# Kernel tuning notes

Measured on AMD Instinct MI355X. Metric: run time of the kernel, lower is better.

## Reference

```python
import jax, jax.numpy as jnp
import numpy as np

B, L, E, H, EXP = 2, 2048, 1024, 16, 4
D = E // H
EPS = 1e-5

def layernorm(x, g, b):
    mu = jnp.mean(x, axis=-1, keepdims=True)
    var = jnp.var(x, axis=-1, keepdims=True)
    return (x - mu) * jax.lax.rsqrt(var + EPS) * g + b

def setup_inputs() -> dict:
    key = jax.random.key(0)
    ks = jax.random.split(key, 12)
    s = 0.02
    return {
        "x": jax.random.normal(ks[0], (B, L, E), dtype=jnp.float32),
        "ln1_g": jnp.ones((E,), jnp.float32),
        "ln1_b": jnp.zeros((E,), jnp.float32),
        "W_qkv": jax.random.normal(ks[1], (E, 3 * E), dtype=jnp.float32) * s,
        "W_proj": jax.random.normal(ks[2], (E, E), dtype=jnp.float32) * s,
        "b_proj": jnp.zeros((E,), jnp.float32),
        "ln2_g": jnp.ones((E,), jnp.float32),
        "ln2_b": jnp.zeros((E,), jnp.float32),
        "W1": jax.random.normal(ks[3], (E, EXP * E), dtype=jnp.float32) * s,
        "b1": jnp.zeros((EXP * E,), jnp.float32),
        "W2": jax.random.normal(ks[4], (EXP * E, E), dtype=jnp.float32) * s,
        "b2": jnp.zeros((E,), jnp.float32),
    }

def reference(x, ln1_g, ln1_b, W_qkv, W_proj, b_proj, ln2_g, ln2_b, W1, b1, W2, b2):
    # --- attention sub-block (pre-LN) ---
    h = layernorm(x, ln1_g, ln1_b)                      # [B,L,E]
    qkv = h @ W_qkv                                      # [B,L,3E]
    q, k, v = jnp.split(qkv, 3, axis=-1)
    q = q.reshape(B, L, H, D).transpose(0, 2, 1, 3)      # [B,H,L,D]
    k = k.reshape(B, L, H, D).transpose(0, 2, 1, 3)
    v = v.reshape(B, L, H, D).transpose(0, 2, 1, 3)
    scale = jnp.sqrt(jnp.float32(E))                     # NOTE: module divides by sqrt(E), not sqrt(D)
    att = jnp.einsum('bhqd,bhkd->bhqk', q, k) / scale
    att = jax.nn.softmax(att, axis=-1)
    out = jnp.einsum('bhqk,bhkd->bhqd', att, v)          # [B,H,L,D]
    out = out.transpose(0, 2, 1, 3).reshape(B, L, E)
    x = x + out @ W_proj + b_proj                         # residual
    # --- feed-forward sub-block (pre-LN) ---
    h = layernorm(x, ln2_g, ln2_b)
    h = jax.nn.gelu(h @ W1 + b1, approximate=False)       # torch GELU is exact erf
    x = x + h @ W2 + b2
    return x
```

## Files before the change

### kernel.cpp

```cpp
#include <hip/hip_runtime.h>
#include <cstdint>
#include <cstddef>


typedef __bf16 bht;
typedef __attribute__((ext_vector_type(8))) __bf16 bf16x8;
typedef __attribute__((ext_vector_type(4))) __bf16 bf16x4;
typedef __attribute__((ext_vector_type(4))) float f32x4;
typedef __attribute__((ext_vector_type(4))) short short4v;

#define B_ 2
#define L_ 2048
#define E_ 1024
#define H_ 16
#define D_ 64
#define ROWS_ (B_ * L_)

#define QSCALE_ 0.045084441f

__device__ __forceinline__ void glds16(const void* g, void* l) {
    __builtin_amdgcn_global_load_lds(
        (const __attribute__((address_space(1))) unsigned int*)g,
        (__attribute__((address_space(3))) unsigned int*)l, 16, 0, 0);
}

__device__ __forceinline__ short4v as_s4(bf16x4 v) {
    return __builtin_bit_cast(short4v, v);
}

__global__ __launch_bounds__(256)
void transpose_cast(const float* __restrict__ in, bht* __restrict__ out, int R, int C) {
    __shared__ float tile[32][33];
    const int bx = blockIdx.x * 32;
    const int by = blockIdx.y * 32;
    const int tx = threadIdx.x, ty = threadIdx.y;
    #pragma unroll
    for (int i = 0; i < 32; i += 8)
        tile[ty + i][tx] = in[(size_t)(by + ty + i) * C + bx + tx];
    __syncthreads();
    #pragma unroll
    for (int i = 0; i < 32; i += 8)
        out[(size_t)(bx + ty + i) * R + by + tx] = (bht)tile[tx][ty + i];
}

__global__ __launch_bounds__(256)
void ln_kernel(const float* __restrict__ x, const float* __restrict__ g,
               const float* __restrict__ b, bht* __restrict__ out) {
    const int row = blockIdx.x, t = threadIdx.x;
    const float4 v = ((const float4*)(x + (size_t)row * E_))[t];
    float s  = v.x + v.y + v.z + v.w;
    float ss = v.x*v.x + v.y*v.y + v.z*v.z + v.w*v.w;
    #pragma unroll
    for (int off = 32; off > 0; off >>= 1) {
        s  += __shfl_down(s, off);
        ss += __shfl_down(ss, off);
    }
    __shared__ float red[8];
    const int wave = t >> 6, lane = t & 63;
    if (lane == 0) { red[wave] = s; red[4 + wave] = ss; }
    __syncthreads();
    s  = red[0] + red[1] + red[2] + red[3];
    ss = red[4] + red[5] + red[6] + red[7];
    const float mean = s * (1.0f / (float)E_);
    const float var  = ss * (1.0f / (float)E_) - mean * mean;
    const float rstd = rsqrtf(var + 1e-5f);
    const float4 gv = ((const float4*)g)[t];
    const float4 bv = ((const float4*)b)[t];
    bf16x4 o;
    o.x = (bht)((v.x - mean) * rstd * gv.x + bv.x);
    o.y = (bht)((v.y - mean) * rstd * gv.y + bv.y);
    o.z = (bht)((v.z - mean) * rstd * gv.z + bv.z);
    o.w = (bht)((v.w - mean) * rstd * gv.w + bv.w);
    *(bf16x4*)(out + (size_t)row * E_ + t * 4) = o;
}

enum { EPI_QKV = 0, EPI_RESID = 1, EPI_GELU = 2 };

template <int EPI>
__global__ __launch_bounds__(256)
void gemm_bt(const bht* __restrict__ A, const bht* __restrict__ Bt,
             const float* __restrict__ bias, const float* __restrict__ resid,
             void* __restrict__ outp,
             bht* __restrict__ qo, bht* __restrict__ ko, bht* __restrict__ vto,
             int M, int N, int K) {
    __shared__ __align__(16) char smem[33792];
    bht* As = (bht*)smem;
    bht* Bs = (bht*)(smem + 16384);
    const int t = threadIdx.x;
    const int lane = t & 63, wave = t >> 6;
    const int lane15 = lane & 15, quad = lane >> 4;
    const int waveM = wave >> 1, waveN = wave & 1;
    const int bm = blockIdx.y * 128, bn = blockIdx.x * 128;

    f32x4 acc[4][4];
    #pragma unroll
    for (int i = 0; i < 4; ++i)
        #pragma unroll
        for (int j = 0; j < 4; ++j)
            acc[i][j] = f32x4{0.f, 0.f, 0.f, 0.f};

    const int swz = lane15 & 7;

    for (int k0 = 0; k0 < K; k0 += 64) {
        #pragma unroll
        for (int i = 0; i < 4; ++i) {
            const int g = i * 256 + t;
            const int row = g >> 3;
            const int col = ((g & 7) ^ (row & 7)) * 8;
            glds16(A  + (size_t)(bm + row) * K + k0 + col, (char*)As + (size_t)g * 16);
            glds16(Bt + (size_t)(bn + row) * K + k0 + col, (char*)Bs + (size_t)g * 16);
        }
        __syncthreads();
        #pragma unroll
        for (int kk = 0; kk < 2; ++kk) {
            const int pc = ((kk * 4 + quad) ^ swz) * 8;
            bf16x8 af[4], bfv[4];
            #pragma unroll
            for (int i = 0; i < 4; ++i)
                af[i] = *(const bf16x8*)(As + (waveM * 64 + i * 16 + lane15) * 64 + pc);
            #pragma unroll
            for (int j = 0; j < 4; ++j)
                bfv[j] = *(const bf16x8*)(Bs + (waveN * 64 + j * 16 + lane15) * 64 + pc);
            #pragma unroll
            for (int i = 0; i < 4; ++i)
                #pragma unroll
                for (int j = 0; j < 4; ++j)
                    acc[i][j] = __builtin_amdgcn_mfma_f32_16x16x32_bf16(af[i], bfv[j], acc[i][j], 0, 0, 0);
        }
        __syncthreads();
    }

    if constexpr (EPI == EPI_QKV) {
        if (bn >= 2048) {
            bht* Vtile = (bht*)smem;
            #pragma unroll
            for (int i = 0; i < 4; ++i) {
                const int rl0 = waveM * 64 + i * 16 + quad * 4;
                #pragma unroll
                for (int j = 0; j < 4; ++j) {
                    const int cl = waveN * 64 + j * 16 + lane15;
                    #pragma unroll
                    for (int r = 0; r < 4; ++r)
                        Vtile[(size_t)cl * 132 + rl0 + r] = (bht)acc[i][j][r];
                }
            }
            __syncthreads();
            const int b = bm >> 11;
            const int l0 = bm & 2047;
            #pragma unroll
            for (int it = 0; it < 8; ++it) {
                const int row = it * 16 + (t >> 4);
                const int ch  = t & 15;
                const int cg = (bn - 2048) + row;
                const int h = cg >> 6, d = cg & 63;
                const int bh = b * H_ + h;
                *(bf16x8*)(vto + ((size_t)bh * D_ + d) * L_ + l0 + ch * 8) =
                    *(const bf16x8*)(Vtile + (size_t)row * 132 + ch * 8);
            }
        } else {
            #pragma unroll
            for (int i = 0; i < 4; ++i) {
                const int row0 = bm + waveM * 64 + i * 16 + quad * 4;
                #pragma unroll
                for (int j = 0; j < 4; ++j) {
                    const int col = bn + waveN * 64 + j * 16 + lane15;
                    const int seg = col >> 10;
                    const int c = col & 1023;
                    const int h = c >> 6, d = c & 63;
                    #pragma unroll
                    for (int r = 0; r < 4; ++r) {
                        const int m = row0 + r;
                        const int b = m >> 11, l = m & 2047;
                        const int bh = b * H_ + h;
                        const float v = acc[i][j][r];
                        if (seg == 0)
                            qo[((size_t)bh * L_ + l) * D_ + d] = (bht)(v * QSCALE_);
                        else
                            ko[((size_t)bh * L_ + l) * D_ + d] = (bht)v;
                    }
                }
            }
        }
    } else {
        #pragma unroll
        for (int i = 0; i < 4; ++i) {
            const int row0 = bm + waveM * 64 + i * 16 + quad * 4;
            #pragma unroll
            for (int j = 0; j < 4; ++j) {
                const int col = bn + waveN * 64 + j * 16 + lane15;
                #pragma unroll
                for (int r = 0; r < 4; ++r) {
                    const int m = row0 + r;
                    float v = acc[i][j][r];
                    if (EPI == EPI_RESID) {
                        ((float*)outp)[(size_t)m * N + col] =
                            v + bias[col] + resid[(size_t)m * N + col];
                    } else {
                        v += bias[col];
                        v = 0.5f * v * (1.0f + erff(v * 0.70710678118654752f));
                        ((bht*)outp)[(size_t)m * N + col] = (bht)v;
                    }
                }
            }
        }
    }
}

template <int EPI>
__global__ __launch_bounds__(256)
void gemm_bt64(const bht* __restrict__ A, const bht* __restrict__ Bt,
               const float* __restrict__ bias, const float* __restrict__ resid,
               void* __restrict__ outp, int M, int N, int K) {
    __shared__ __align__(16) bht As[64 * 64];
    __shared__ __align__(16) bht Bs[128 * 64];
    const int t = threadIdx.x;
    const int lane = t & 63, wave = t >> 6;
    const int lane15 = lane & 15, quad = lane >> 4;
    const int waveM = wave >> 1, waveN = wave & 1;
    const int bm = blockIdx.y * 64, bn = blockIdx.x * 128;

    f32x4 acc[2][4];
    #pragma unroll
    for (int i = 0; i < 2; ++i)
        #pragma unroll
        for (int j = 0; j < 4; ++j)
            acc[i][j] = f32x4{0.f, 0.f, 0.f, 0.f};

    const int swz = lane15 & 7;

    for (int k0 = 0; k0 < K; k0 += 64) {
        #pragma unroll
        for (int i = 0; i < 2; ++i) {
            const int g = i * 256 + t;
            const int row = g >> 3;
            const int col = ((g & 7) ^ (row & 7)) * 8;
            glds16(A + (size_t)(bm + row) * K + k0 + col, (char*)As + (size_t)g * 16);
        }
        #pragma unroll
        for (int i = 0; i < 4; ++i) {
            const int g = i * 256 + t;
            const int row = g >> 3;
            const int col = ((g & 7) ^ (row & 7)) * 8;
            glds16(Bt + (size_t)(bn + row) * K + k0 + col, (char*)Bs + (size_t)g * 16);
        }
        __syncthreads();
        #pragma unroll
        for (int kk = 0; kk < 2; ++kk) {
            const int pc = ((kk * 4 + quad) ^ swz) * 8;
            bf16x8 af[2], bfv[4];
            #pragma unroll
            for (int i = 0; i < 2; ++i)
                af[i] = *(const bf16x8*)(As + (waveM * 32 + i * 16 + lane15) * 64 + pc);
            #pragma unroll
            for (int j = 0; j < 4; ++j)
                bfv[j] = *(const bf16x8*)(Bs + (waveN * 64 + j * 16 + lane15) * 64 + pc);
            #pragma unroll
            for (int i = 0; i < 2; ++i)
                #pragma unroll
                for (int j = 0; j < 4; ++j)
                    acc[i][j] = __builtin_amdgcn_mfma_f32_16x16x32_bf16(af[i], bfv[j], acc[i][j], 0, 0, 0);
        }
        __syncthreads();
    }

    #pragma unroll
    for (int i = 0; i < 2; ++i) {
        const int row0 = bm + waveM * 32 + i * 16 + quad * 4;
        #pragma unroll
        for (int j = 0; j < 4; ++j) {
            const int col = bn + waveN * 64 + j * 16 + lane15;
            #pragma unroll
            for (int r = 0; r < 4; ++r) {
                const int m = row0 + r;
                float v = acc[i][j][r];
                if (EPI == EPI_RESID) {
                    ((float*)outp)[(size_t)m * N + col] =
                        v + bias[col] + resid[(size_t)m * N + col];
                } else {
                    v += bias[col];
                    v = 0.5f * v * (1.0f + erff(v * 0.70710678118654752f));
                    ((bht*)outp)[(size_t)m * N + col] = (bht)v;
                }
            }
        }
    }
}

#define KT_ 128

__global__ __launch_bounds__(256)
void attn_kernel(const bht* __restrict__ Q, const bht* __restrict__ Kb,
                 const bht* __restrict__ Vt, bht* __restrict__ O) {
    __shared__ __align__(16) bht Ks[KT_ * 64];
    __shared__ __align__(16) bht Vs[64 * KT_];
    __shared__ float Ls[4][16];
    const int t = threadIdx.x;
    const int lane = t & 63, wave = t >> 6;
    const int lane15 = lane & 15, quad = lane >> 4;
    const int bh = blockIdx.x, qt = blockIdx.y;

    const bht* Qh = Q  + (size_t)bh * L_ * D_;
    const bht* Kh = Kb + (size_t)bh * L_ * D_;
    const bht* Vh = Vt + (size_t)bh * D_ * L_;

    const int q0 = qt * 64 + wave * 16;

    bf16x8 aq[2];
    #pragma unroll
    for (int kc = 0; kc < 2; ++kc)
        aq[kc] = *(const bf16x8*)(Qh + (size_t)(q0 + lane15) * D_ + kc * 32 + quad * 8);

    f32x4 o_acc[4];
    #pragma unroll
    for (int db = 0; db < 4; ++db) o_acc[db] = f32x4{0.f, 0.f, 0.f, 0.f};
    float l_sum = 0.f;

    const int pc0 = (quad ^ (lane15 & 7)) * 8;
    const int pc1 = pc0 ^ 32;

    for (int kt = 0; kt < L_ / KT_; ++kt) {
        const int key0 = kt * KT_;
        #pragma unroll
        for (int i = 0; i < 4; ++i) {
            const int g = i * 256 + t;
            const int krow = g >> 3;
            const int ksc = ((g & 7) ^ (krow & 7)) * 8;
            glds16(Kh + (size_t)(key0 + krow) * D_ + ksc, (char*)Ks + (size_t)g * 16);
        }
        #pragma unroll
        for (int i = 0; i < 4; ++i) {
            const int g = i * 256 + t;
            const int vrow = g >> 4;
            const int vsc = ((g & 15) ^ (vrow & 7)) * 8;
            glds16(Vh + (size_t)vrow * L_ + key0 + vsc, (char*)Vs + (size_t)g * 16);
        }
        __syncthreads();

        #pragma unroll
        for (int nb = 0; nb < 8; ++nb) {
            const bf16x8 ak0 = *(const bf16x8*)(Ks + (nb * 16 + lane15) * 64 + pc0);
            const bf16x8 ak1 = *(const bf16x8*)(Ks + (nb * 16 + lane15) * 64 + pc1);
            f32x4 st = __builtin_amdgcn_mfma_f32_16x16x32_bf16(
                ak0, aq[0], f32x4{0.f, 0.f, 0.f, 0.f}, 0, 0, 0);
            st = __builtin_amdgcn_mfma_f32_16x16x32_bf16(ak1, aq[1], st, 0, 0, 0);
            bf16x4 pk;
            #pragma unroll
            for (int r = 0; r < 4; ++r) {
                const float pv = exp2f(st[r]);
                l_sum += pv;
                pk[r] = (bht)pv;
            }
            const short4v pf = as_s4(pk);
            #pragma unroll
            for (int db = 0; db < 4; ++db) {
                const int row = db * 16 + lane15;
                const int c16 = (nb * 2 + (quad >> 1)) ^ (row & 7);
                const bf16x4 bv = *(const bf16x4*)(Vs + row * KT_ + c16 * 8 + (quad & 1) * 4);
                o_acc[db] = __builtin_amdgcn_mfma_f32_16x16x16bf16_1k(
                    pf, as_s4(bv), o_acc[db], 0, 0, 0);
            }
        }
        __syncthreads();
    }

    l_sum += __shfl_xor(l_sum, 16);
    l_sum += __shfl_xor(l_sum, 32);
    Ls[wave][lane15] = l_sum;
    asm volatile("s_waitcnt lgkmcnt(0)" ::: "memory");

    const int b = bh >> 4, h = bh & 15;
    #pragma unroll
    for (int r = 0; r < 4; ++r) {
        const int l = q0 + quad * 4 + r;
        const float inv = 1.0f / Ls[wave][quad * 4 + r];
        #pragma unroll
        for (int db = 0; db < 4; ++db)
            O[((size_t)b * L_ + l) * E_ + h * 64 + db * 16 + lane15] =
                (bht)(o_acc[db][r] * inv);
    }
}

extern "C" void kernel_launch(void* const* d_in, const int* in_sizes, int n_in,
                              void* d_out, int out_size, void* d_ws, size_t ws_size,
                              hipStream_t stream) {
    const float* x      = (const float*)d_in[0];
    const float* ln1_g  = (const float*)d_in[1];
    const float* ln1_b  = (const float*)d_in[2];
    const float* W_qkv  = (const float*)d_in[3];
    const float* W_proj = (const float*)d_in[4];
    const float* b_proj = (const float*)d_in[5];
    const float* ln2_g  = (const float*)d_in[6];
    const float* ln2_b  = (const float*)d_in[7];
    const float* W1     = (const float*)d_in[8];
    const float* b1     = (const float*)d_in[9];
    const float* W2     = (const float*)d_in[10];
    const float* b2     = (const float*)d_in[11];
    float* out = (float*)d_out;

    char* ws = (char*)d_ws;
    auto alloc = [&](size_t bytes) {
        char* p = ws;
        ws += (bytes + 255) & ~(size_t)255;
        return p;
    };
    bht*   WqkvT  = (bht*)alloc((size_t)3072 * 1024 * 2);
    bht*   WprojT = (bht*)alloc((size_t)1024 * 1024 * 2);
    bht*   W1T    = (bht*)alloc((size_t)4096 * 1024 * 2);
    bht*   W2T    = (bht*)alloc((size_t)1024 * 4096 * 2);
    bht*   hb     = (bht*)alloc((size_t)ROWS_ * E_ * 2);
    float* x1     = (float*)alloc((size_t)ROWS_ * E_ * 4);
    bht*   Qb     = (bht*)alloc((size_t)B_ * H_ * L_ * D_ * 2);
    bht*   Kbuf   = (bht*)alloc((size_t)B_ * H_ * L_ * D_ * 2);
    bht*   Vtb    = (bht*)alloc((size_t)B_ * H_ * D_ * L_ * 2);
    bht*   attno  = (bht*)alloc((size_t)ROWS_ * E_ * 2);
    bht*   ffn1   = Qb;

    transpose_cast<<<dim3(3072 / 32, 1024 / 32), dim3(32, 8), 0, stream>>>(W_qkv, WqkvT, 1024, 3072);
    transpose_cast<<<dim3(1024 / 32, 1024 / 32), dim3(32, 8), 0, stream>>>(W_proj, WprojT, 1024, 1024);
    transpose_cast<<<dim3(4096 / 32, 1024 / 32), dim3(32, 8), 0, stream>>>(W1, W1T, 1024, 4096);
    transpose_cast<<<dim3(1024 / 32, 4096 / 32), dim3(32, 8), 0, stream>>>(W2, W2T, 4096, 1024);

    ln_kernel<<<ROWS_, 256, 0, stream>>>(x, ln1_g, ln1_b, hb);

    gemm_bt<EPI_QKV><<<dim3(3072 / 128, ROWS_ / 128), 256, 0, stream>>>(
        hb, WqkvT, nullptr, nullptr, nullptr, Qb, Kbuf, Vtb, ROWS_, 3072, 1024);

    attn_kernel<<<dim3(B_ * H_, L_ / 64), 256, 0, stream>>>(Qb, Kbuf, Vtb, attno);

    gemm_bt64<EPI_RESID><<<dim3(1024 / 128, ROWS_ / 64), 256, 0, stream>>>(
        attno, WprojT, b_proj, x, x1, ROWS_, 1024, 1024);

    ln_kernel<<<ROWS_, 256, 0, stream>>>(x1, ln2_g, ln2_b, hb);

    gemm_bt<EPI_GELU><<<dim3(4096 / 128, ROWS_ / 128), 256, 0, stream>>>(
        hb, W1T, b1, nullptr, ffn1, nullptr, nullptr, nullptr, ROWS_, 4096, 1024);

    gemm_bt64<EPI_RESID><<<dim3(1024 / 128, ROWS_ / 64), 256, 0, stream>>>(
        ffn1, W2T, b2, x1, out, ROWS_, 1024, 4096);

    (void)in_sizes; (void)n_in; (void)out_size; (void)ws_size;
}
```

Measured before the change: 388.6 us.

## Overlap next K/V tile loads with attention compute and swizzle V halves

Splits each attention key tile into a QK/softmax phase and a PV phase. The next K tile is prefetched while PV runs and the next V tile while the following QK phase runs, with explicit waitcnt/barriers and raised wave priority around the MFMA sections. The V-transpose store swaps 4-element halves for half the threads and the PV read applies a matching XOR on the half offset, to reduce LDS bank conflicts. This adds more barriers per tile and holds 8 packed P fragments in registers, which raises register pressure.

```diff
diff --git a/kernel.cpp b/kernel.cpp
--- a/kernel.cpp
+++ b/kernel.cpp
@@ -154,8 +154,10 @@
                 const int cg = (bn - 2048) + row;
                 const int h = cg >> 6, d = cg & 63;
                 const int bh = b * H_ + h;
-                *(bf16x8*)(vto + ((size_t)bh * D_ + d) * L_ + l0 + ch * 8) =
-                    *(const bf16x8*)(Vtile + (size_t)row * 132 + ch * 8);
+                bf16x8 vv = *(const bf16x8*)(Vtile + (size_t)row * 132 + ch * 8);
+                if (t & 128)
+                    vv = __builtin_shufflevector(vv, vv, 4, 5, 6, 7, 0, 1, 2, 3);
+                *(bf16x8*)(vto + ((size_t)bh * D_ + d) * L_ + l0 + ch * 8) = vv;
             }
         } else {
             #pragma unroll
@@ -287,6 +289,7 @@
 }
 
 #define KT_ 128
+#define NT_ (L_ / KT_)
 
 __global__ __launch_bounds__(256)
 void attn_kernel(const bht* __restrict__ Q, const bht* __restrict__ Kb,
@@ -317,9 +320,10 @@
 
     const int pc0 = (quad ^ (lane15 & 7)) * 8;
     const int pc1 = pc0 ^ 32;
-
-    for (int kt = 0; kt < L_ / KT_; ++kt) {
-        const int key0 = kt * KT_;
+    const int vhalf4 = ((quad & 1) ^ ((lane15 >> 3) & 1)) * 4;
+
+    auto stageK = [&](int kt2) {
+        const int key0 = kt2 * KT_;
         #pragma unroll
         for (int i = 0; i < 4; ++i) {
             const int g = i * 256 + t;
@@ -327,6 +331,9 @@
             const int ksc = ((g & 7) ^ (krow & 7)) * 8;
             glds16(Kh + (size_t)(key0 + krow) * D_ + ksc, (char*)Ks + (size_t)g * 16);
         }
+    };
+    auto stageV = [&](int kt2) {
+        const int key0 = kt2 * KT_;
         #pragma unroll
         for (int i = 0; i < 4; ++i) {
             const int g = i * 256 + t;
@@ -334,8 +341,17 @@
             const int vsc = ((g & 15) ^ (vrow & 7)) * 8;
             glds16(Vh + (size_t)vrow * L_ + key0 + vsc, (char*)Vs + (size_t)g * 16);
         }
-        __syncthreads();
-
+    };
+
+    stageK(0);
+    stageV(0);
+
+    for (int kt = 0; kt < NT_; ++kt) {
+        asm volatile("s_waitcnt vmcnt(4) lgkmcnt(0)" ::: "memory");
+        __builtin_amdgcn_s_barrier();
+
+        __builtin_amdgcn_s_setprio(1);
+        short4v pk[8];
         #pragma unroll
         for (int nb = 0; nb < 8; ++nb) {
             const bf16x8 ak0 = *(const bf16x8*)(Ks + (nb * 16 + lane15) * 64 + pc0);
@@ -343,24 +359,38 @@
             f32x4 st = __builtin_amdgcn_mfma_f32_16x16x32_bf16(
                 ak0, aq[0], f32x4{0.f, 0.f, 0.f, 0.f}, 0, 0, 0);
             st = __builtin_amdgcn_mfma_f32_16x16x32_bf16(ak1, aq[1], st, 0, 0, 0);
-            bf16x4 pk;
+            bf16x4 pkv;
             #pragma unroll
             for (int r = 0; r < 4; ++r) {
                 const float pv = exp2f(st[r]);
                 l_sum += pv;
-                pk[r] = (bht)pv;
-            }
-            const short4v pf = as_s4(pk);
+                pkv[r] = (bht)pv;
+            }
+            pk[nb] = as_s4(pkv);
+        }
+        __builtin_amdgcn_s_setprio(0);
+
+        asm volatile("s_waitcnt vmcnt(0) lgkmcnt(0)" ::: "memory");
+        __builtin_amdgcn_s_barrier();
+        if (kt + 1 < NT_) stageK(kt + 1);
+
+        __builtin_amdgcn_s_setprio(1);
+        #pragma unroll
+        for (int nb = 0; nb < 8; ++nb) {
             #pragma unroll
             for (int db = 0; db < 4; ++db) {
                 const int row = db * 16 + lane15;
                 const int c16 = (nb * 2 + (quad >> 1)) ^ (row & 7);
-                const bf16x4 bv = *(const bf16x4*)(Vs + row * KT_ + c16 * 8 + (quad & 1) * 4);
+                const bf16x4 bv = *(const bf16x4*)(Vs + row * KT_ + c16 * 8 + vhalf4);
                 o_acc[db] = __builtin_amdgcn_mfma_f32_16x16x16bf16_1k(
-                    pf, as_s4(bv), o_acc[db], 0, 0, 0);
-            }
-        }
-        __syncthreads();
+                    pk[nb], as_s4(bv), o_acc[db], 0, 0, 0);
+            }
+        }
+        __builtin_amdgcn_s_setprio(0);
+
+        asm volatile("s_waitcnt lgkmcnt(0)" ::: "memory");
+        __builtin_amdgcn_s_barrier();
+        if (kt + 1 < NT_) stageV(kt + 1);
     }
 
     l_sum += __shfl_xor(l_sum, 16);
```

Result: no change. 382.0 us (-1.7%).
